# Performance work log

Measured on AMD Instinct MI355X. Metric: run time of the kernel, lower is better.

Reference implementation:

```python
import jax, jax.numpy as jnp
import numpy as np

B, T, D, H, C, WIN = 2, 2048, 512, 8, 64, 128
EPS = 1e-6


def _rms_norm(x, w):
    # x: (..., C)
    norm = jax.lax.rsqrt(jnp.mean(x * x, axis=-1, keepdims=True) + EPS)
    return x * norm * w


def _apply_rope(x, cos_p, sin_p):
    # x: (B, H, T, C); cos_p/sin_p: (T, C)
    half = x.shape[-1] // 2
    x1, x2 = x[..., :half], x[..., half:]
    rotated = jnp.concatenate([-x2, x1], axis=-1)
    return x * cos_p + rotated * sin_p


def setup_inputs() -> dict:
    key = jax.random.key(0)
    ks = jax.random.split(key, 5)
    h = jax.random.normal(ks[0], (B, T, D), dtype=jnp.float32)
    # RoPE cache (rotate-half convention): (T_max, head_dim)
    inv_freq = 1.0 / (10000.0 ** (jnp.arange(0, C, 2, dtype=jnp.float32) / C))  # (C/2,)
    pos = jnp.arange(T, dtype=jnp.float32)
    freqs = pos[:, None] * inv_freq[None, :]                      # (T, C/2)
    emb = jnp.concatenate([freqs, freqs], axis=-1)                # (T, C)
    rope_cos = jnp.cos(emb)
    rope_sin = jnp.sin(emb)
    scale = 0.02
    W_q = jax.random.normal(ks[1], (D, H * C), dtype=jnp.float32) * scale
    W_k = jax.random.normal(ks[2], (D, H * C), dtype=jnp.float32) * scale
    W_v = jax.random.normal(ks[3], (D, H * C), dtype=jnp.float32) * scale
    W_o = jax.random.normal(ks[4], (H * C, D), dtype=jnp.float32) * scale
    q_norm_w = jnp.ones((C,), dtype=jnp.float32)
    k_norm_w = jnp.ones((C,), dtype=jnp.float32)
    return {"h": h, "rope_cos": rope_cos, "rope_sin": rope_sin,
            "W_q": W_q, "W_k": W_k, "W_v": W_v, "W_o": W_o,
            "q_norm_w": q_norm_w, "k_norm_w": k_norm_w}


def reference(h, rope_cos, rope_sin, W_q, W_k, W_v, W_o, q_norm_w, k_norm_w):
    Bx, Tx, _ = h.shape
    q = (h @ W_q).reshape(Bx, Tx, H, C)
    k = (h @ W_k).reshape(Bx, Tx, H, C)
    v = (h @ W_v).reshape(Bx, Tx, H, C)
    q = _rms_norm(q, q_norm_w)
    k = _rms_norm(k, k_norm_w)
    positions = jnp.arange(Tx)
    cos_p = rope_cos[positions]   # (T, C)
    sin_p = rope_sin[positions]
    # transpose to (B, H, T, C), apply rope, transpose back handled implicitly
    q = _apply_rope(q.transpose(0, 2, 1, 3), cos_p, sin_p).transpose(0, 2, 1, 3)
    k = _apply_rope(k.transpose(0, 2, 1, 3), cos_p, sin_p).transpose(0, 2, 1, 3)
    i = positions[:, None]
    j = positions[None, :]
    sw_mask = (j <= i) & (j > i - WIN)                # (T, T) banded causal
    logits = jnp.einsum('bthc,bshc->bhts', q, k) / np.sqrt(C).astype(np.float32)
    logits = jnp.where(sw_mask[None, None], logits, jnp.float32(-jnp.inf))
    attn = jax.nn.softmax(logits, axis=-1)
    out = jnp.einsum('bhts,bshc->bthc', attn, v).reshape(Bx, Tx, H * C)
    return out @ W_o
```

## Files before the change

kernel.cpp:

```cpp
#include <hip/hip_runtime.h>
#include <hip/hip_bf16.h>
#include <cmath>

#define Bb 2
#define Tt 2048
#define Dd 512
#define Hh 8
#define Cc 64
#define WINw 128

using u16x8 = __attribute__((ext_vector_type(8))) unsigned short;
using s16x8 = __attribute__((ext_vector_type(8))) short;
using f32x4 = __attribute__((ext_vector_type(4))) float;

__device__ __forceinline__ float bf2f(unsigned short u) {
  union { unsigned int i; float f; } v; v.i = ((unsigned int)u) << 16; return v.f;
}
__device__ __forceinline__ unsigned short f2bf(float f) {
  __hip_bfloat16 b = __float2bfloat16(f);
  return *reinterpret_cast<unsigned short*>(&b);
}

__global__ __launch_bounds__(256) void transpose512(
    const float* __restrict__ src, unsigned short* __restrict__ dst) {
  __shared__ unsigned short tile[64 * 65];
  int n0 = blockIdx.x * 64, k0 = blockIdx.y * 64;
  int tx = threadIdx.x, ty = threadIdx.y;
  #pragma unroll
  for (int i = 0; i < 16; ++i) {
    int k = ty * 16 + i;
    tile[k * 65 + tx] = f2bf(src[(k0 + k) * 512 + n0 + tx]);
  }
  __syncthreads();
  #pragma unroll
  for (int i = 0; i < 16; ++i) {
    int n = ty * 16 + i;
    dst[(n0 + n) * 512 + k0 + tx] = tile[tx * 65 + n];
  }
}

__global__ __launch_bounds__(256) void qkv_gemm(
    const float* __restrict__ Hm,
    const unsigned short* __restrict__ WT,
    const float* __restrict__ normw,
    const float* __restrict__ rcos,
    const float* __restrict__ rsin,
    unsigned short* __restrict__ Out,
    int do_rope) {
  __shared__ alignas(16) unsigned short Al[64 * 72];
  __shared__ alignas(16) unsigned short Bl[64 * 72];
  int m0 = blockIdx.x * 64;
  int head = blockIdx.y;
  int n0 = head * 64;
  int tid = threadIdx.x;
  int wave = tid >> 6, lane = tid & 63;
  int ln = lane & 15, qd = lane >> 4;
  int lrow = tid >> 2;
  int lcol = (tid & 3) * 16;

  f32x4 acc[4] = {f32x4{0,0,0,0}, f32x4{0,0,0,0}, f32x4{0,0,0,0}, f32x4{0,0,0,0}};

  for (int k0 = 0; k0 < 512; k0 += 64) {
    const float4* ga = (const float4*)&Hm[(m0 + lrow) * 512 + k0 + lcol];
    float4 f0 = ga[0], f1 = ga[1], f2 = ga[2], f3 = ga[3];
    const u16x8* gb = (const u16x8*)&WT[(n0 + lrow) * 512 + k0 + lcol];
    u16x8 b0 = gb[0], b1 = gb[1];
    u16x8 c0 = {f2bf(f0.x), f2bf(f0.y), f2bf(f0.z), f2bf(f0.w),
                f2bf(f1.x), f2bf(f1.y), f2bf(f1.z), f2bf(f1.w)};
    u16x8 c1 = {f2bf(f2.x), f2bf(f2.y), f2bf(f2.z), f2bf(f2.w),
                f2bf(f3.x), f2bf(f3.y), f2bf(f3.z), f2bf(f3.w)};
    *(u16x8*)&Al[lrow * 72 + lcol] = c0;
    *(u16x8*)&Al[lrow * 72 + lcol + 8] = c1;
    *(u16x8*)&Bl[lrow * 72 + lcol] = b0;
    *(u16x8*)&Bl[lrow * 72 + lcol + 8] = b1;
    __syncthreads();
    #pragma unroll
    for (int kk = 0; kk < 64; kk += 32) {
      s16x8 af = *(const s16x8*)&Al[(wave * 16 + ln) * 72 + kk + qd * 8];
      #pragma unroll
      for (int nt = 0; nt < 4; ++nt) {
        s16x8 bfm = *(const s16x8*)&Bl[(nt * 16 + ln) * 72 + kk + qd * 8];
        acc[nt] = __builtin_amdgcn_mfma_f32_16x16x32_bf16(af, bfm, acc[nt], 0, 0, 0);
      }
    }
    __syncthreads();
  }

  float vals[4][4];
  #pragma unroll
  for (int nt = 0; nt < 4; ++nt)
    #pragma unroll
    for (int r = 0; r < 4; ++r) vals[nt][r] = acc[nt][r];

  if (do_rope) {
    #pragma unroll
    for (int r = 0; r < 4; ++r) {
      float ss = 0.f;
      #pragma unroll
      for (int nt = 0; nt < 4; ++nt) ss += vals[nt][r] * vals[nt][r];
      ss += __shfl_xor(ss, 1, 64);
      ss += __shfl_xor(ss, 2, 64);
      ss += __shfl_xor(ss, 4, 64);
      ss += __shfl_xor(ss, 8, 64);
      float nrm = rsqrtf(ss * (1.0f / 64.0f) + 1e-6f);
      #pragma unroll
      for (int nt = 0; nt < 4; ++nt) vals[nt][r] *= nrm;
    }
    #pragma unroll
    for (int nt = 0; nt < 4; ++nt) {
      float w = normw[nt * 16 + ln];
      #pragma unroll
      for (int r = 0; r < 4; ++r) vals[nt][r] *= w;
    }
    float res[4][4];
    #pragma unroll
    for (int r = 0; r < 4; ++r) {
      int row = m0 + wave * 16 + qd * 4 + r;
      int t = row & (Tt - 1);
      #pragma unroll
      for (int nt = 0; nt < 4; ++nt) {
        int c = nt * 16 + ln;
        float cs = rcos[t * 64 + c];
        float sn = rsin[t * 64 + c];
        float part = vals[nt ^ 2][r];
        float rot = (nt < 2) ? -part : part;
        res[nt][r] = vals[nt][r] * cs + rot * sn;
      }
    }
    #pragma unroll
    for (int nt = 0; nt < 4; ++nt)
      #pragma unroll
      for (int r = 0; r < 4; ++r) vals[nt][r] = res[nt][r];
  }

  #pragma unroll
  for (int r = 0; r < 4; ++r) {
    int row = m0 + wave * 16 + qd * 4 + r;
    int b = row >> 11, t = row & (Tt - 1);
    unsigned short* op = &Out[((b * Hh + head) * Tt + t) * 64 + ln];
    #pragma unroll
    for (int nt = 0; nt < 4; ++nt) op[nt * 16] = f2bf(vals[nt][r]);
  }
}

__global__ __launch_bounds__(256) void attn_mfma(
    const unsigned short* __restrict__ Q,
    const unsigned short* __restrict__ K,
    const unsigned short* __restrict__ V,
    unsigned short* __restrict__ AO) {
  __shared__ alignas(16) unsigned short Ql[64 * 72];
  __shared__ alignas(16) unsigned short KP[192 * 72];
  __shared__ alignas(16) unsigned short Vt[64 * 200];

  int tid = threadIdx.x;
  int wave = tid >> 6, lane = tid & 63;
  int ln = lane & 15, qd = lane >> 4;
  int qtile = blockIdx.x, bh = blockIdx.y;
  int t0 = qtile * 64;
  int kb = t0 - 128;

  const unsigned short* Qg = Q + ((size_t)bh * Tt + t0) * 64;
  const unsigned short* Kg = K + (size_t)bh * Tt * 64;
  const unsigned short* Vg = V + (size_t)bh * Tt * 64;

  int srow = tid >> 2;
  int scol = (tid & 3) * 16;

  {
    const u16x8* g = (const u16x8*)&Qg[srow * 64 + scol];
    u16x8 a0 = g[0], a1 = g[1];
    *(u16x8*)&Ql[srow * 72 + scol] = a0;
    *(u16x8*)&Ql[srow * 72 + scol + 8] = a1;
  }
  #pragma unroll
  for (int p = 0; p < 3; ++p) {
    int row = p * 64 + srow;
    int kg = kb + row; if (kg < 0) kg = 0;
    const u16x8* gk = (const u16x8*)&Kg[kg * 64 + scol];
    u16x8 k0 = gk[0], k1 = gk[1];
    const u16x8* gv = (const u16x8*)&Vg[kg * 64 + scol];
    u16x8 v0 = gv[0], v1 = gv[1];
    *(u16x8*)&KP[row * 72 + scol] = k0;
    *(u16x8*)&KP[row * 72 + scol + 8] = k1;
    #pragma unroll
    for (int j = 0; j < 8; ++j) {
      Vt[(scol + j) * 200 + row] = v0[j];
      Vt[(scol + 8 + j) * 200 + row] = v1[j];
    }
  }
  __syncthreads();

  int q0 = wave * 16;
  s16x8 aq0 = *(const s16x8*)&Ql[(q0 + ln) * 72 + qd * 8];
  s16x8 aq1 = *(const s16x8*)&Ql[(q0 + ln) * 72 + 32 + qd * 8];
  f32x4 sf[12];
  #pragma unroll
  for (int nt = 0; nt < 12; ++nt) {
    s16x8 b0 = *(const s16x8*)&KP[(nt * 16 + ln) * 72 + qd * 8];
    s16x8 b1 = *(const s16x8*)&KP[(nt * 16 + ln) * 72 + 32 + qd * 8];
    f32x4 acc = {0.f, 0.f, 0.f, 0.f};
    acc = __builtin_amdgcn_mfma_f32_16x16x32_bf16(aq0, b0, acc, 0, 0, 0);
    acc = __builtin_amdgcn_mfma_f32_16x16x32_bf16(aq1, b1, acc, 0, 0, 0);
    sf[nt] = acc;
  }
  __syncthreads();

  unsigned short* Pl = KP;
  int ok0 = (t0 < 128) ? (128 - t0) : 0;
  #pragma unroll
  for (int r = 0; r < 4; ++r) {
    int lq = q0 + qd * 4 + r;
    float mx = -INFINITY;
    #pragma unroll
    for (int nt = 0; nt < 12; ++nt) {
      int kk = nt * 16 + ln;
      bool valid = (kk > lq) && (kk <= lq + 128) && (kk >= ok0);
      float s = valid ? sf[nt][r] * 0.125f : -INFINITY;
      sf[nt][r] = s;
      mx = fmaxf(mx, s);
    }
    mx = fmaxf(mx, __shfl_xor(mx, 1, 64));
    mx = fmaxf(mx, __shfl_xor(mx, 2, 64));
    mx = fmaxf(mx, __shfl_xor(mx, 4, 64));
    mx = fmaxf(mx, __shfl_xor(mx, 8, 64));
    float sum = 0.f;
    #pragma unroll
    for (int nt = 0; nt < 12; ++nt) {
      float e = __expf(sf[nt][r] - mx);
      sf[nt][r] = e;
      sum += e;
    }
    sum += __shfl_xor(sum, 1, 64);
    sum += __shfl_xor(sum, 2, 64);
    sum += __shfl_xor(sum, 4, 64);
    sum += __shfl_xor(sum, 8, 64);
    float inv = 1.0f / sum;
    #pragma unroll
    for (int nt = 0; nt < 12; ++nt)
      Pl[lq * 200 + nt * 16 + ln] = f2bf(sf[nt][r] * inv);
  }
  __syncthreads();

  f32x4 oa[4] = {f32x4{0,0,0,0}, f32x4{0,0,0,0}, f32x4{0,0,0,0}, f32x4{0,0,0,0}};
  #pragma unroll
  for (int s = 0; s < 6; ++s) {
    s16x8 ap = *(const s16x8*)&Pl[(q0 + ln) * 200 + s * 32 + qd * 8];
    #pragma unroll
    for (int nt = 0; nt < 4; ++nt) {
      s16x8 bv = *(const s16x8*)&Vt[(nt * 16 + ln) * 200 + s * 32 + qd * 8];
      oa[nt] = __builtin_amdgcn_mfma_f32_16x16x32_bf16(ap, bv, oa[nt], 0, 0, 0);
    }
  }

  int b = bh >> 3, h = bh & 7;
  #pragma unroll
  for (int r = 0; r < 4; ++r) {
    int t = t0 + q0 + qd * 4 + r;
    unsigned short* op = &AO[(((size_t)b * Tt + t) * Hh + h) * 64 + ln];
    #pragma unroll
    for (int nt = 0; nt < 4; ++nt) op[nt * 16] = f2bf(oa[nt][r]);
  }
}

__global__ __launch_bounds__(256) void out_gemm(
    const unsigned short* __restrict__ Am,
    const unsigned short* __restrict__ WT,
    float* __restrict__ Out) {
  __shared__ alignas(16) unsigned short Al[64 * 72];
  __shared__ alignas(16) unsigned short Bl[64 * 72];
  int m0 = blockIdx.x * 64;
  int n0 = blockIdx.y * 64;
  int tid = threadIdx.x;
  int wave = tid >> 6, lane = tid & 63;
  int ln = lane & 15, qd = lane >> 4;
  int lrow = tid >> 2;
  int lcol = (tid & 3) * 16;

  f32x4 acc[4] = {f32x4{0,0,0,0}, f32x4{0,0,0,0}, f32x4{0,0,0,0}, f32x4{0,0,0,0}};

  for (int k0 = 0; k0 < 512; k0 += 64) {
    const u16x8* ga = (const u16x8*)&Am[(m0 + lrow) * 512 + k0 + lcol];
    u16x8 a0 = ga[0], a1 = ga[1];
    const u16x8* gb = (const u16x8*)&WT[(n0 + lrow) * 512 + k0 + lcol];
    u16x8 b0 = gb[0], b1 = gb[1];
    *(u16x8*)&Al[lrow * 72 + lcol] = a0;
    *(u16x8*)&Al[lrow * 72 + lcol + 8] = a1;
    *(u16x8*)&Bl[lrow * 72 + lcol] = b0;
    *(u16x8*)&Bl[lrow * 72 + lcol + 8] = b1;
    __syncthreads();
    #pragma unroll
    for (int kk = 0; kk < 64; kk += 32) {
      s16x8 af = *(const s16x8*)&Al[(wave * 16 + ln) * 72 + kk + qd * 8];
      #pragma unroll
      for (int nt = 0; nt < 4; ++nt) {
        s16x8 bfm = *(const s16x8*)&Bl[(nt * 16 + ln) * 72 + kk + qd * 8];
        acc[nt] = __builtin_amdgcn_mfma_f32_16x16x32_bf16(af, bfm, acc[nt], 0, 0, 0);
      }
    }
    __syncthreads();
  }

  #pragma unroll
  for (int r = 0; r < 4; ++r) {
    int row = m0 + wave * 16 + qd * 4 + r;
    #pragma unroll
    for (int nt = 0; nt < 4; ++nt)
      Out[row * 512 + n0 + nt * 16 + ln] = acc[nt][r];
  }
}

extern "C" void kernel_launch(void* const* d_in, const int* in_sizes, int n_in,
                              void* d_out, int out_size, void* d_ws, size_t ws_size,
                              hipStream_t stream) {
  const float* h   = (const float*)d_in[0];
  const float* rc  = (const float*)d_in[1];
  const float* rs  = (const float*)d_in[2];
  const float* Wq  = (const float*)d_in[3];
  const float* Wk  = (const float*)d_in[4];
  const float* Wv  = (const float*)d_in[5];
  const float* Wo  = (const float*)d_in[6];
  const float* qnw = (const float*)d_in[7];
  const float* knw = (const float*)d_in[8];

  unsigned short* ws  = (unsigned short*)d_ws;
  unsigned short* WTq = ws;
  unsigned short* WTk = WTq + 512 * 512;
  unsigned short* WTv = WTk + 512 * 512;
  unsigned short* WTo = WTv + 512 * 512;
  unsigned short* Qw  = WTo + 512 * 512;
  unsigned short* Kw  = Qw + 2097152;
  unsigned short* Vw  = Kw + 2097152;
  unsigned short* AOw = Vw + 2097152;

  dim3 tb(64, 4);
  transpose512<<<dim3(8, 8), tb, 0, stream>>>(Wq, WTq);
  transpose512<<<dim3(8, 8), tb, 0, stream>>>(Wk, WTk);
  transpose512<<<dim3(8, 8), tb, 0, stream>>>(Wv, WTv);
  transpose512<<<dim3(8, 8), tb, 0, stream>>>(Wo, WTo);

  qkv_gemm<<<dim3(64, 8), 256, 0, stream>>>(h, WTq, qnw, rc, rs, Qw, 1);
  qkv_gemm<<<dim3(64, 8), 256, 0, stream>>>(h, WTk, knw, rc, rs, Kw, 1);
  qkv_gemm<<<dim3(64, 8), 256, 0, stream>>>(h, WTv, nullptr, nullptr, nullptr, Vw, 0);

  attn_mfma<<<dim3(32, 16), 256, 0, stream>>>(Qw, Kw, Vw, AOw);

  out_gemm<<<dim3(64, 8), 256, 0, stream>>>(AOw, WTo, (float*)d_out);
}
```

Measured before the change: 131.1 us.

## Fuse QKV projections into one 128x128-tiled GEMM and batch weight transposes

Converts h to bf16 once in a separate kernel and merges the four weight transposes into a single launch. The three Q/K/V GEMMs become one launch over a concatenated weight matrix with 128x128 tiles and a 2x2 wave layout, and each wave picks its output buffer and whether to apply norm/RoPE from its head index. The output GEMM also moves to 128x128 tiles. This cuts launch count and redundant h conversion and improves register-level reuse, but it reduces grid size (384 and 128 blocks), which may underfill the GPU's compute units.

```diff
diff --git a/kernel.cpp b/kernel.cpp
--- a/kernel.cpp
+++ b/kernel.cpp
@@ -21,9 +21,24 @@
   return *reinterpret_cast<unsigned short*>(&b);
 }
 
-__global__ __launch_bounds__(256) void transpose512(
+__global__ __launch_bounds__(256) void cvt_f32_bf16(
     const float* __restrict__ src, unsigned short* __restrict__ dst) {
+  size_t i = ((size_t)blockIdx.x * 256 + threadIdx.x) * 8;
+  const float4* g = (const float4*)&src[i];
+  float4 f0 = g[0], f1 = g[1];
+  u16x8 o = {f2bf(f0.x), f2bf(f0.y), f2bf(f0.z), f2bf(f0.w),
+             f2bf(f1.x), f2bf(f1.y), f2bf(f1.z), f2bf(f1.w)};
+  *(u16x8*)&dst[i] = o;
+}
+
+__global__ __launch_bounds__(256) void transpose_all(
+    const float* __restrict__ s0, const float* __restrict__ s1,
+    const float* __restrict__ s2, const float* __restrict__ s3,
+    unsigned short* __restrict__ d) {
   __shared__ unsigned short tile[64 * 65];
+  const float* srcs[4] = {s0, s1, s2, s3};
+  const float* src = srcs[blockIdx.z];
+  unsigned short* dst = d + (size_t)blockIdx.z * 512 * 512;
   int n0 = blockIdx.x * 64, k0 = blockIdx.y * 64;
   int tx = threadIdx.x, ty = threadIdx.y;
   #pragma unroll
@@ -39,107 +54,125 @@
   }
 }
 
-__global__ __launch_bounds__(256) void qkv_gemm(
-    const float* __restrict__ Hm,
-    const unsigned short* __restrict__ WT,
-    const float* __restrict__ normw,
-    const float* __restrict__ rcos,
-    const float* __restrict__ rsin,
-    unsigned short* __restrict__ Out,
-    int do_rope) {
-  __shared__ alignas(16) unsigned short Al[64 * 72];
-  __shared__ alignas(16) unsigned short Bl[64 * 72];
-  int m0 = blockIdx.x * 64;
-  int head = blockIdx.y;
-  int n0 = head * 64;
+__global__ __launch_bounds__(256) void qkv_fused(
+    const unsigned short* __restrict__ Hb,
+    const unsigned short* __restrict__ WTall,
+    const float* __restrict__ qnw, const float* __restrict__ knw,
+    const float* __restrict__ rcos, const float* __restrict__ rsin,
+    unsigned short* __restrict__ Qw, unsigned short* __restrict__ Kw,
+    unsigned short* __restrict__ Vw) {
+  __shared__ alignas(16) unsigned short Al[128 * 72];
+  __shared__ alignas(16) unsigned short Bl[128 * 72];
+  int m0 = blockIdx.x * 128;
+  int n0 = blockIdx.y * 128;
   int tid = threadIdx.x;
   int wave = tid >> 6, lane = tid & 63;
   int ln = lane & 15, qd = lane >> 4;
-  int lrow = tid >> 2;
-  int lcol = (tid & 3) * 16;
-
-  f32x4 acc[4] = {f32x4{0,0,0,0}, f32x4{0,0,0,0}, f32x4{0,0,0,0}, f32x4{0,0,0,0}};
+  int wm = wave >> 1, wn = wave & 1;
+  int srow = tid >> 2, scol = (tid & 3) * 16;
+
+  f32x4 acc[4][4];
+  #pragma unroll
+  for (int mi = 0; mi < 4; ++mi)
+    #pragma unroll
+    for (int ni = 0; ni < 4; ++ni) acc[mi][ni] = f32x4{0.f, 0.f, 0.f, 0.f};
 
   for (int k0 = 0; k0 < 512; k0 += 64) {
-    const float4* ga = (const float4*)&Hm[(m0 + lrow) * 512 + k0 + lcol];
-    float4 f0 = ga[0], f1 = ga[1], f2 = ga[2], f3 = ga[3];
-    const u16x8* gb = (const u16x8*)&WT[(n0 + lrow) * 512 + k0 + lcol];
-    u16x8 b0 = gb[0], b1 = gb[1];
-    u16x8 c0 = {f2bf(f0.x), f2bf(f0.y), f2bf(f0.z), f2bf(f0.w),
-                f2bf(f1.x), f2bf(f1.y), f2bf(f1.z), f2bf(f1.w)};
-    u16x8 c1 = {f2bf(f2.x), f2bf(f2.y), f2bf(f2.z), f2bf(f2.w),
-                f2bf(f3.x), f2bf(f3.y), f2bf(f3.z), f2bf(f3.w)};
-    *(u16x8*)&Al[lrow * 72 + lcol] = c0;
-    *(u16x8*)&Al[lrow * 72 + lcol + 8] = c1;
-    *(u16x8*)&Bl[lrow * 72 + lcol] = b0;
-    *(u16x8*)&Bl[lrow * 72 + lcol + 8] = b1;
+    #pragma unroll
+    for (int p = 0; p < 2; ++p) {
+      int row = p * 64 + srow;
+      const u16x8* ga = (const u16x8*)&Hb[(size_t)(m0 + row) * 512 + k0 + scol];
+      u16x8 a0 = ga[0], a1 = ga[1];
+      const u16x8* gb = (const u16x8*)&WTall[(size_t)(n0 + row) * 512 + k0 + scol];
+      u16x8 b0 = gb[0], b1 = gb[1];
+      *(u16x8*)&Al[row * 72 + scol] = a0;
+      *(u16x8*)&Al[row * 72 + scol + 8] = a1;
+      *(u16x8*)&Bl[row * 72 + scol] = b0;
+      *(u16x8*)&Bl[row * 72 + scol + 8] = b1;
+    }
     __syncthreads();
     #pragma unroll
     for (int kk = 0; kk < 64; kk += 32) {
-      s16x8 af = *(const s16x8*)&Al[(wave * 16 + ln) * 72 + kk + qd * 8];
-      #pragma unroll
-      for (int nt = 0; nt < 4; ++nt) {
-        s16x8 bfm = *(const s16x8*)&Bl[(nt * 16 + ln) * 72 + kk + qd * 8];
-        acc[nt] = __builtin_amdgcn_mfma_f32_16x16x32_bf16(af, bfm, acc[nt], 0, 0, 0);
+      s16x8 af[4], bfr[4];
+      #pragma unroll
+      for (int mi = 0; mi < 4; ++mi)
+        af[mi] = *(const s16x8*)&Al[(wm * 64 + mi * 16 + ln) * 72 + kk + qd * 8];
+      #pragma unroll
+      for (int ni = 0; ni < 4; ++ni)
+        bfr[ni] = *(const s16x8*)&Bl[(wn * 64 + ni * 16 + ln) * 72 + kk + qd * 8];
+      #pragma unroll
+      for (int mi = 0; mi < 4; ++mi)
+        #pragma unroll
+        for (int ni = 0; ni < 4; ++ni)
+          acc[mi][ni] = __builtin_amdgcn_mfma_f32_16x16x32_bf16(
+              af[mi], bfr[ni], acc[mi][ni], 0, 0, 0);
+    }
+    __syncthreads();
+  }
+
+  int gh = blockIdx.y * 2 + wn;
+  int mat = gh >> 3, head = gh & 7;
+  unsigned short* Out = (mat == 0) ? Qw : (mat == 1) ? Kw : Vw;
+  const float* nw = (mat == 0) ? qnw : knw;
+  bool do_rope = (mat < 2);
+
+  #pragma unroll
+  for (int mi = 0; mi < 4; ++mi) {
+    float vals[4][4];
+    #pragma unroll
+    for (int ni = 0; ni < 4; ++ni)
+      #pragma unroll
+      for (int r = 0; r < 4; ++r) vals[ni][r] = acc[mi][ni][r];
+
+    if (do_rope) {
+      #pragma unroll
+      for (int r = 0; r < 4; ++r) {
+        float ss = 0.f;
+        #pragma unroll
+        for (int ni = 0; ni < 4; ++ni) ss += vals[ni][r] * vals[ni][r];
+        ss += __shfl_xor(ss, 1, 64);
+        ss += __shfl_xor(ss, 2, 64);
+        ss += __shfl_xor(ss, 4, 64);
+        ss += __shfl_xor(ss, 8, 64);
+        float nrm = rsqrtf(ss * (1.0f / 64.0f) + 1e-6f);
+        #pragma unroll
+        for (int ni = 0; ni < 4; ++ni) vals[ni][r] *= nrm;
       }
-    }
-    __syncthreads();
-  }
-
-  float vals[4][4];
-  #pragma unroll
-  for (int nt = 0; nt < 4; ++nt)
-    #pragma unroll
-    for (int r = 0; r < 4; ++r) vals[nt][r] = acc[nt][r];
-
-  if (do_rope) {
+      #pragma unroll
+      for (int ni = 0; ni < 4; ++ni) {
+        float w = nw[ni * 16 + ln];
+        #pragma unroll
+        for (int r = 0; r < 4; ++r) vals[ni][r] *= w;
+      }
+      float res[4][4];
+      #pragma unroll
+      for (int r = 0; r < 4; ++r) {
+        int row = m0 + wm * 64 + mi * 16 + qd * 4 + r;
+        int t = row & (Tt - 1);
+        #pragma unroll
+        for (int ni = 0; ni < 4; ++ni) {
+          int c = ni * 16 + ln;
+          float cs = rcos[t * 64 + c];
+          float sn = rsin[t * 64 + c];
+          float part = vals[ni ^ 2][r];
+          float rot = (ni < 2) ? -part : part;
+          res[ni][r] = vals[ni][r] * cs + rot * sn;
+        }
+      }
+      #pragma unroll
+      for (int ni = 0; ni < 4; ++ni)
+        #pragma unroll
+        for (int r = 0; r < 4; ++r) vals[ni][r] = res[ni][r];
+    }
+
     #pragma unroll
     for (int r = 0; r < 4; ++r) {
-      float ss = 0.f;
-      #pragma unroll
-      for (int nt = 0; nt < 4; ++nt) ss += vals[nt][r] * vals[nt][r];
-      ss += __shfl_xor(ss, 1, 64);
-      ss += __shfl_xor(ss, 2, 64);
-      ss += __shfl_xor(ss, 4, 64);
-      ss += __shfl_xor(ss, 8, 64);
-      float nrm = rsqrtf(ss * (1.0f / 64.0f) + 1e-6f);
-      #pragma unroll
-      for (int nt = 0; nt < 4; ++nt) vals[nt][r] *= nrm;
-    }
-    #pragma unroll
-    for (int nt = 0; nt < 4; ++nt) {
-      float w = normw[nt * 16 + ln];
-      #pragma unroll
-      for (int r = 0; r < 4; ++r) vals[nt][r] *= w;
-    }
-    float res[4][4];
-    #pragma unroll
-    for (int r = 0; r < 4; ++r) {
-      int row = m0 + wave * 16 + qd * 4 + r;
-      int t = row & (Tt - 1);
-      #pragma unroll
-      for (int nt = 0; nt < 4; ++nt) {
-        int c = nt * 16 + ln;
-        float cs = rcos[t * 64 + c];
-        float sn = rsin[t * 64 + c];
-        float part = vals[nt ^ 2][r];
-        float rot = (nt < 2) ? -part : part;
-        res[nt][r] = vals[nt][r] * cs + rot * sn;
-      }
-    }
-    #pragma unroll
-    for (int nt = 0; nt < 4; ++nt)
-      #pragma unroll
-      for (int r = 0; r < 4; ++r) vals[nt][r] = res[nt][r];
-  }
-
-  #pragma unroll
-  for (int r = 0; r < 4; ++r) {
-    int row = m0 + wave * 16 + qd * 4 + r;
-    int b = row >> 11, t = row & (Tt - 1);
-    unsigned short* op = &Out[((b * Hh + head) * Tt + t) * 64 + ln];
-    #pragma unroll
-    for (int nt = 0; nt < 4; ++nt) op[nt * 16] = f2bf(vals[nt][r]);
+      int row = m0 + wm * 64 + mi * 16 + qd * 4 + r;
+      int b = row >> 11, t = row & (Tt - 1);
+      unsigned short* op = &Out[(((size_t)b * Hh + head) * Tt + t) * 64 + ln];
+      #pragma unroll
+      for (int ni = 0; ni < 4; ++ni) op[ni * 16] = f2bf(vals[ni][r]);
+    }
   }
 }
 
@@ -262,51 +295,68 @@
   }
 }
 
-__global__ __launch_bounds__(256) void out_gemm(
+__global__ __launch_bounds__(256) void out_gemm128(
     const unsigned short* __restrict__ Am,
     const unsigned short* __restrict__ WT,
     float* __restrict__ Out) {
-  __shared__ alignas(16) unsigned short Al[64 * 72];
-  __shared__ alignas(16) unsigned short Bl[64 * 72];
-  int m0 = blockIdx.x * 64;
-  int n0 = blockIdx.y * 64;
+  __shared__ alignas(16) unsigned short Al[128 * 72];
+  __shared__ alignas(16) unsigned short Bl[128 * 72];
+  int m0 = blockIdx.x * 128;
+  int n0 = blockIdx.y * 128;
   int tid = threadIdx.x;
   int wave = tid >> 6, lane = tid & 63;
   int ln = lane & 15, qd = lane >> 4;
-  int lrow = tid >> 2;
-  int lcol = (tid & 3) * 16;
-
-  f32x4 acc[4] = {f32x4{0,0,0,0}, f32x4{0,0,0,0}, f32x4{0,0,0,0}, f32x4{0,0,0,0}};
+  int wm = wave >> 1, wn = wave & 1;
+  int srow = tid >> 2, scol = (tid & 3) * 16;
+
+  f32x4 acc[4][4];
+  #pragma unroll
+  for (int mi = 0; mi < 4; ++mi)
+    #pragma unroll
+    for (int ni = 0; ni < 4; ++ni) acc[mi][ni] = f32x4{0.f, 0.f, 0.f, 0.f};
 
   for (int k0 = 0; k0 < 512; k0 += 64) {
-    const u16x8* ga = (const u16x8*)&Am[(m0 + lrow) * 512 + k0 + lcol];
-    u16x8 a0 = ga[0], a1 = ga[1];
-    const u16x8* gb = (const u16x8*)&WT[(n0 + lrow) * 512 + k0 + lcol];
-    u16x8 b0 = gb[0], b1 = gb[1];
-    *(u16x8*)&Al[lrow * 72 + lcol] = a0;
-    *(u16x8*)&Al[lrow * 72 + lcol + 8] = a1;
-    *(u16x8*)&Bl[lrow * 72 + lcol] = b0;
-    *(u16x8*)&Bl[lrow * 72 + lcol + 8] = b1;
+    #pragma unroll
+    for (int p = 0; p < 2; ++p) {
+      int row = p * 64 + srow;
+      const u16x8* ga = (const u16x8*)&Am[(size_t)(m0 + row) * 512 + k0 + scol];
+      u16x8 a0 = ga[0], a1 = ga[1];
+      const u16x8* gb = (const u16x8*)&WT[(size_t)(n0 + row) * 512 + k0 + scol];
+      u16x8 b0 = gb[0], b1 = gb[1];
+      *(u16x8*)&Al[row * 72 + scol] = a0;
+      *(u16x8*)&Al[row * 72 + scol + 8] = a1;
+      *(u16x8*)&Bl[row * 72 + scol] = b0;
+      *(u16x8*)&Bl[row * 72 + scol + 8] = b1;
+    }
     __syncthreads();
     #pragma unroll
     for (int kk = 0; kk < 64; kk += 32) {
-      s16x8 af = *(const s16x8*)&Al[(wave * 16 + ln) * 72 + kk + qd * 8];
-      #pragma unroll
-      for (int nt = 0; nt < 4; ++nt) {
-        s16x8 bfm = *(const s16x8*)&Bl[(nt * 16 + ln) * 72 + kk + qd * 8];
-        acc[nt] = __builtin_amdgcn_mfma_f32_16x16x32_bf16(af, bfm, acc[nt], 0, 0, 0);
-      }
+      s16x8 af[4], bfr[4];
+      #pragma unroll
+      for (int mi = 0; mi < 4; ++mi)
+        af[mi] = *(const s16x8*)&Al[(wm * 64 + mi * 16 + ln) * 72 + kk + qd * 8];
+      #pragma unroll
+      for (int ni = 0; ni < 4; ++ni)
+        bfr[ni] = *(const s16x8*)&Bl[(wn * 64 + ni * 16 + ln) * 72 + kk + qd * 8];
+      #pragma unroll
+      for (int mi = 0; mi < 4; ++mi)
+        #pragma unroll
+        for (int ni = 0; ni < 4; ++ni)
+          acc[mi][ni] = __builtin_amdgcn_mfma_f32_16x16x32_bf16(
+              af[mi], bfr[ni], acc[mi][ni], 0, 0, 0);
     }
     __syncthreads();
   }
 
   #pragma unroll
-  for (int r = 0; r < 4; ++r) {
-    int row = m0 + wave * 16 + qd * 4 + r;
-    #pragma unroll
-    for (int nt = 0; nt < 4; ++nt)
-      Out[row * 512 + n0 + nt * 16 + ln] = acc[nt][r];
-  }
+  for (int mi = 0; mi < 4; ++mi)
+    #pragma unroll
+    for (int r = 0; r < 4; ++r) {
+      int row = m0 + wm * 64 + mi * 16 + qd * 4 + r;
+      #pragma unroll
+      for (int ni = 0; ni < 4; ++ni)
+        Out[(size_t)row * 512 + n0 + wn * 64 + ni * 16 + ln] = acc[mi][ni][r];
+    }
 }
 
 extern "C" void kernel_launch(void* const* d_in, const int* in_sizes, int n_in,
@@ -322,27 +372,22 @@
   const float* qnw = (const float*)d_in[7];
   const float* knw = (const float*)d_in[8];
 
-  unsigned short* ws  = (unsigned short*)d_ws;
-  unsigned short* WTq = ws;
-  unsigned short* WTk = WTq + 512 * 512;
-  unsigned short* WTv = WTk + 512 * 512;
-  unsigned short* WTo = WTv + 512 * 512;
-  unsigned short* Qw  = WTo + 512 * 512;
-  unsigned short* Kw  = Qw + 2097152;
-  unsigned short* Vw  = Kw + 2097152;
-  unsigned short* AOw = Vw + 2097152;
-
-  dim3 tb(64, 4);
-  transpose512<<<dim3(8, 8), tb, 0, stream>>>(Wq, WTq);
-  transpose512<<<dim3(8, 8), tb, 0, stream>>>(Wk, WTk);
-  transpose512<<<dim3(8, 8), tb, 0, stream>>>(Wv, WTv);
-  transpose512<<<dim3(8, 8), tb, 0, stream>>>(Wo, WTo);
-
-  qkv_gemm<<<dim3(64, 8), 256, 0, stream>>>(h, WTq, qnw, rc, rs, Qw, 1);
-  qkv_gemm<<<dim3(64, 8), 256, 0, stream>>>(h, WTk, knw, rc, rs, Kw, 1);
-  qkv_gemm<<<dim3(64, 8), 256, 0, stream>>>(h, WTv, nullptr, nullptr, nullptr, Vw, 0);
+  unsigned short* ws    = (unsigned short*)d_ws;
+  unsigned short* WTall = ws;
+  unsigned short* WTo   = WTall + 1536 * 512;
+  unsigned short* Hb    = WTo + 512 * 512;
+  unsigned short* Qw    = Hb + 2097152;
+  unsigned short* Kw    = Qw + 2097152;
+  unsigned short* Vw    = Kw + 2097152;
+  unsigned short* AOw   = Vw + 2097152;
+
+  cvt_f32_bf16<<<1024, 256, 0, stream>>>(h, Hb);
+  transpose_all<<<dim3(8, 8, 4), dim3(64, 4), 0, stream>>>(Wq, Wk, Wv, Wo, WTall);
+
+  qkv_fused<<<dim3(32, 12), 256, 0, stream>>>(Hb, WTall, qnw, knw, rc, rs,
+                                              Qw, Kw, Vw);
 
   attn_mfma<<<dim3(32, 16), 256, 0, stream>>>(Qw, Kw, Vw, AOw);
 
-  out_gemm<<<dim3(64, 8), 256, 0, stream>>>(AOw, WTo, (float*)d_out);
-}
+  out_gemm128<<<dim3(32, 4), 256, 0, stream>>>(AOw, WTo, (float*)d_out);
+}
```

After: 116.9 us. 10.8% less time.
